# Kernel tuning notes

Hardware: AMD Instinct MI355X
Metric: run time of the kernel (lower is better)

The kernel has to match this reference:

```python
import jax, jax.numpy as jnp
import numpy as np

LATENT = 1024
HIDDEN = 4096
ENC = 1024
HEADS = 16
HEAD_DIM = LATENT // HEADS
B, SQ, SK = 4, 1024, 1024
EPS = 1e-5


def _linear(x, w, b):
    # torch nn.Linear: y = x @ w.T + b, w shape (out, in)
    return jnp.einsum('bsi,oi->bso', x, w) + b


def _mha(Q, K, wq, bq, wk, bk, wv, bv, wo, bo):
    Bq, Sq, _ = Q.shape
    Sk = K.shape[1]
    Qp = _linear(Q, wq, bq).reshape(Bq, Sq, HEADS, HEAD_DIM)
    Kp = _linear(K, wk, bk).reshape(Bq, Sk, HEADS, HEAD_DIM)
    Vp = _linear(K, wv, bv).reshape(Bq, Sk, HEADS, HEAD_DIM)
    # NOTE: original scales by 1/sqrt(latent_size), not 1/sqrt(head_dim)
    E = jnp.einsum('bqhd,bkhd->bhqk', Qp, Kp) / np.sqrt(LATENT).astype(np.float32)
    A = jax.nn.softmax(E, axis=-1)
    O = jnp.einsum('bhqk,bkhd->bqhd', A, Vp).reshape(Bq, Sq, LATENT)
    return _linear(O, wo, bo)


def _ln(x, g, b):
    mu = jnp.mean(x, axis=-1, keepdims=True)
    var = jnp.mean((x - mu) ** 2, axis=-1, keepdims=True)
    return (x - mu) * jax.lax.rsqrt(var + EPS) * g + b


def setup_inputs() -> dict:
    key = jax.random.key(0)
    ks = jax.random.split(key, 32)
    s = 0.02
    d = {
        'Q': jax.random.normal(ks[0], (B, SQ, LATENT), jnp.float32),
        'K': jax.random.normal(ks[1], (B, SK, ENC), jnp.float32),
        'a1_wq': jax.random.normal(ks[2], (LATENT, LATENT)) * s,
        'a1_bq': jnp.zeros((LATENT,)),
        'a1_wk': jax.random.normal(ks[3], (LATENT, LATENT)) * s,
        'a1_bk': jnp.zeros((LATENT,)),
        'a1_wv': jax.random.normal(ks[4], (LATENT, LATENT)) * s,
        'a1_bv': jnp.zeros((LATENT,)),
        'a1_wo': jax.random.normal(ks[5], (LATENT, LATENT)) * s,
        'a1_bo': jnp.zeros((LATENT,)),
        'a2_wq': jax.random.normal(ks[6], (LATENT, LATENT)) * s,
        'a2_bq': jnp.zeros((LATENT,)),
        'a2_wk': jax.random.normal(ks[7], (LATENT, ENC)) * s,
        'a2_bk': jnp.zeros((LATENT,)),
        'a2_wv': jax.random.normal(ks[8], (LATENT, ENC)) * s,
        'a2_bv': jnp.zeros((LATENT,)),
        'a2_wo': jax.random.normal(ks[9], (LATENT, LATENT)) * s,
        'a2_bo': jnp.zeros((LATENT,)),
        'fc_w1': jax.random.normal(ks[10], (HIDDEN, LATENT)) * s,
        'fc_b1': jnp.zeros((HIDDEN,)),
        'fc_w2': jax.random.normal(ks[11], (LATENT, HIDDEN)) * s,
        'fc_b2': jnp.zeros((LATENT,)),
        'ln0_g': jnp.ones((LATENT,)), 'ln0_b': jnp.zeros((LATENT,)),
        'ln1_g': jnp.ones((LATENT,)), 'ln1_b': jnp.zeros((LATENT,)),
        'ln2_g': jnp.ones((LATENT,)), 'ln2_b': jnp.zeros((LATENT,)),
    }
    return d


def reference(Q, K, a1_wq, a1_bq, a1_wk, a1_bk, a1_wv, a1_bv, a1_wo, a1_bo,
              a2_wq, a2_bq, a2_wk, a2_bk, a2_wv, a2_bv, a2_wo, a2_bo,
              fc_w1, fc_b1, fc_w2, fc_b2,
              ln0_g, ln0_b, ln1_g, ln1_b, ln2_g, ln2_b):
    # self-attention block
    A1 = _mha(Q, Q, a1_wq, a1_bq, a1_wk, a1_bk, a1_wv, a1_bv, a1_wo, a1_bo)
    X = _ln(Q + A1, ln0_g, ln0_b)
    # cross-attention block
    A2 = _mha(X, K, a2_wq, a2_bq, a2_wk, a2_bk, a2_wv, a2_bv, a2_wo, a2_bo)
    X = _ln(X + A2, ln1_g, ln1_b)
    # FFN: Linear -> ReLU -> Linear
    FC = _linear(jax.nn.relu(_linear(X, fc_w1, fc_b1)), fc_w2, fc_b2)
    X = _ln(X + FC, ln2_g, ln2_b)
    return X
```

## Files before the change

kernel.cpp:

```cpp
#include <hip/hip_runtime.h>
#include <hip/hip_bf16.h>
#include <math.h>

#define LATENT 1024
#define HIDDEN 4096
#define HEADS 16
#define HEAD_DIM 64
#define BATCH 4
#define SQL 1024
#define SKL 1024

typedef __bf16 bf16;
typedef __attribute__((ext_vector_type(4))) __bf16 bf16x4;
typedef __attribute__((ext_vector_type(8))) __bf16 bf16x8;
typedef __attribute__((ext_vector_type(4))) float f32x4;

#define MFMA16 __builtin_amdgcn_mfma_f32_16x16x32_bf16

__device__ __forceinline__ void async_ld16(const bf16* g, bf16* l) {
    __builtin_amdgcn_global_load_lds(
        (const __attribute__((address_space(1))) unsigned int*)g,
        (__attribute__((address_space(3))) unsigned int*)l,
        16, 0, 0);
}

__global__ void detect_dtype(const void* g, int* flag) {
    if (threadIdx.x == 0) *flag = (*(const float*)g == 1.0f) ? 1 : 0;
}

struct CanonArgs {
    const void* src[28];
    bf16* dst[28];
    int n[28];
};

__global__ __launch_bounds__(256) void canonicalize(CanonArgs a, const int* flagp) {
    const int buf = blockIdx.y;
    const int n = a.n[buf];
    const int i0 = (blockIdx.x * 256 + threadIdx.x) * 8;
    if (i0 >= n) return;
    bf16* dst = a.dst[buf];
    if (*flagp) {
        const float* s = (const float*)a.src[buf];
        float4 u0 = *(const float4*)(s + i0);
        float4 u1 = *(const float4*)(s + i0 + 4);
        bf16x8 o;
        o[0] = (bf16)u0.x; o[1] = (bf16)u0.y; o[2] = (bf16)u0.z; o[3] = (bf16)u0.w;
        o[4] = (bf16)u1.x; o[5] = (bf16)u1.y; o[6] = (bf16)u1.z; o[7] = (bf16)u1.w;
        *(bf16x8*)(dst + i0) = o;
    } else {
        *(bf16x8*)(dst + i0) = *(const bf16x8*)((const bf16*)a.src[buf] + i0);
    }
}

template<bool RELU>
__global__ __launch_bounds__(256, 2)
void gemm8(const bf16* __restrict__ A, const bf16* __restrict__ W,
           const bf16* __restrict__ bias,
           bf16* __restrict__ out0, bf16* __restrict__ out1, bf16* __restrict__ outT,
           int M, int N, int K, int nNormal, int ostride) {
    constexpr int AE   = 128 * 32;
    constexpr int BE   = 256 * 32;
    constexpr int BUFE = AE + BE;
    __shared__ alignas(16) bf16 smem[3 * BUFE];
    const int tid  = threadIdx.x;
    const int w    = tid >> 6;
    const int lane = tid & 63;
    const int quad = lane >> 4;
    const int l16  = lane & 15;
    const int wrr  = w >> 1, wcc = w & 1;
    const int nx  = gridDim.x;
    const int nwg = nx * gridDim.y;
    int bid = blockIdx.y * nx + blockIdx.x;
    bid = (bid & 7) * (nwg >> 3) + (bid >> 3);
    const int bm = (bid / nx) * 128;
    const int bn = (bid % nx) * 256;

    f32x4 acc[4][8] = {};

    const bf16* gsrc[6]; int loff[6];
#pragma unroll
    for (int i = 0; i < 6; ++i) {
        const int s = tid + i * 256;
        if (s < 512) {
            const int r = s >> 2, cs = s & 3;
            gsrc[i] = A + (long)(bm + r) * K + ((cs ^ ((r >> 1) & 3)) << 3);
            loff[i] = s * 8;
        } else {
            const int sb = s - 512;
            const int r = sb >> 2, cs = sb & 3;
            gsrc[i] = W + (long)(bn + r) * K + ((cs ^ ((r >> 1) & 3)) << 3);
            loff[i] = AE + sb * 8;
        }
    }

    int offA[4], offB[8];
#pragma unroll
    for (int i = 0; i < 4; ++i) {
        const int r = wrr * 64 + i * 16 + l16;
        offA[i] = r * 32 + ((quad ^ ((r >> 1) & 3)) << 3);
    }
#pragma unroll
    for (int j = 0; j < 8; ++j) {
        const int r = wcc * 128 + j * 16 + l16;
        offB[j] = AE + r * 32 + ((quad ^ ((r >> 1) & 3)) << 3);
    }

#define STAGE_W(dst, tt)                                                       \
    {                                                                          \
        _Pragma("unroll")                                                      \
        for (int i_ = 0; i_ < 6; ++i_)                                         \
            async_ld16(gsrc[i_] + (tt) * 32, (dst) + loff[i_]);                \
    }

    const int NK = K >> 5;
    bf16 *p0 = smem, *p1 = smem + BUFE, *p2 = smem + 2 * BUFE;
    STAGE_W(p0, 0);
    STAGE_W(p1, 1);
    __asm__ volatile("s_waitcnt vmcnt(6)" ::: "memory");
    __builtin_amdgcn_s_barrier();
    __builtin_amdgcn_sched_barrier(0);

    for (int t = 0; t < NK; ++t) {
        if (t + 2 < NK) STAGE_W(p2, t + 2);
        bf16x8 af[4], bfv[8];
#pragma unroll
        for (int i = 0; i < 4; ++i) af[i]  = *(const bf16x8*)&p0[offA[i]];
#pragma unroll
        for (int j = 0; j < 8; ++j) bfv[j] = *(const bf16x8*)&p0[offB[j]];
#pragma unroll
        for (int j = 0; j < 8; ++j)
#pragma unroll
            for (int i = 0; i < 4; ++i)
                acc[i][j] = MFMA16(af[i], bfv[j], acc[i][j], 0, 0, 0);
        if (t + 2 < NK) {
            __asm__ volatile("s_waitcnt vmcnt(6)" ::: "memory");
        } else if (t + 1 < NK) {
            __asm__ volatile("s_waitcnt vmcnt(0)" ::: "memory");
        }
        if (t + 1 < NK) {
            __builtin_amdgcn_s_barrier();
            __builtin_amdgcn_sched_barrier(0);
        }
        bf16* tp = p0; p0 = p1; p1 = p2; p2 = tp;
    }
#undef STAGE_W

    float bvv[8];
#pragma unroll
    for (int j = 0; j < 8; ++j) bvv[j] = (float)bias[bn + wcc * 128 + j * 16 + l16];

    if (bn < nNormal) {
#pragma unroll
        for (int j = 0; j < 8; ++j) {
            const int colj = bn + wcc * 128 + j * 16;
            bf16* basej = out0;
            int cb = colj;
            if (out1 && cb >= 1024) { basej = out1; cb -= 1024; }
#pragma unroll
            for (int i = 0; i < 4; ++i) {
#pragma unroll
                for (int r = 0; r < 4; ++r) {
                    const int row = bm + wrr * 64 + i * 16 + quad * 4 + r;
                    float v = acc[i][j][r] + bvv[j];
                    if (RELU) v = fmaxf(v, 0.f);
                    basej[(long)row * ostride + cb + l16] = (bf16)v;
                }
            }
        }
    } else {
        const int n0v = bn - nNormal;
        __syncthreads();
#pragma unroll
        for (int p = 0; p < 4; ++p) {
            if (p) __syncthreads();
            if (wcc == (p >> 1)) {
#pragma unroll
                for (int i = 0; i < 4; ++i)
#pragma unroll
                    for (int jl = 0; jl < 4; ++jl) {
                        const int j = (p & 1) * 4 + jl;
                        const int colL = jl * 16 + l16;
                        const int rowL = wrr * 64 + i * 16 + quad * 4;
                        bf16x4 pk;
#pragma unroll
                        for (int r = 0; r < 4; ++r) pk[r] = (bf16)(acc[i][j][r] + bvv[j]);
                        *(bf16x4*)&smem[colL * 136 + rowL] = pk;
                    }
            }
            __syncthreads();
#pragma unroll
            for (int k = 0; k < 8; ++k) {
                const int c = tid + k * 256;
                const int rT = c >> 5, ch = c & 31;
                *(bf16x4*)&outT[(long)(n0v + p * 64 + rT) * M + bm + ch * 4] =
                    *(const bf16x4*)&smem[rT * 136 + ch * 4];
            }
        }
    }
}

template<int BN, bool RELU>
__global__ __launch_bounds__(256, 2)
void gemm2(const bf16* __restrict__ A, const bf16* __restrict__ W,
           const bf16* __restrict__ bias,
           bf16* __restrict__ out0, bf16* __restrict__ out1, bf16* __restrict__ outT,
           int M, int N, int K, int nNormal, int ostride) {
    constexpr int WAVES_N = BN / 64;
    constexpr int WAVES_M = 4 / WAVES_N;
    constexpr int WM = 128 / WAVES_M;
    constexpr int MI = WM / 16;
    constexpr int BROWS = BN / 4;
    constexpr int BUFSZ = (128 + BN) * 64;
    __shared__ alignas(16) bf16 smem[2 * BUFSZ];
    const int tid  = threadIdx.x;
    const int w    = tid >> 6;
    const int lane = tid & 63;
    const int quad = lane >> 4;
    const int l16  = lane & 15;
    const int bm = blockIdx.y * 128;
    const int bn = blockIdx.x * BN;
    const int wr = w / WAVES_N, wc = w % WAVES_N;

    f32x4 acc[MI][4] = {};

    const int srow = lane >> 3;
    const int schk = (lane & 7) * 8;
    const bf16* Abase = A + (long)(bm + w * 32 + srow) * K + schk;
    const bf16* Wbase = W + (long)(bn + w * BROWS + srow) * K + schk;
    const int lAoff = (w * 32 + srow) * 64 + schk;
    const int lBoff = 128 * 64 + (w * BROWS + srow) * 64 + schk;

#define STAGE_G(bufp, kk)                                                      \
    {                                                                          \
        bf16* bb_ = smem + (bufp) * BUFSZ;                                     \
        _Pragma("unroll")                                                      \
        for (int i_ = 0; i_ < 4; ++i_)                                         \
            async_ld16(Abase + (kk) + (long)(i_ * 8) * K, bb_ + lAoff + i_ * 8 * 64); \
        _Pragma("unroll")                                                      \
        for (int i_ = 0; i_ < BROWS / 8; ++i_)                                 \
            async_ld16(Wbase + (kk) + (long)(i_ * 8) * K, bb_ + lBoff + i_ * 8 * 64); \
    }

    STAGE_G(0, 0);
    __asm__ volatile("s_waitcnt vmcnt(0)" ::: "memory");
    __builtin_amdgcn_s_barrier();
    __builtin_amdgcn_sched_barrier(0);

    int cur = 0;
    for (int k0 = 0; k0 < K; k0 += 64) {
        if (k0 + 64 < K) STAGE_G(cur ^ 1, k0 + 64);
        const bf16* lA = smem + cur * BUFSZ;
        const bf16* lB = lA + 128 * 64;
#pragma unroll
        for (int ks = 0; ks < 2; ++ks) {
            bf16x8 af[MI], bfv[4];
#pragma unroll
            for (int i = 0; i < MI; ++i)
                af[i] = *(const bf16x8*)&lA[(wr * WM + i * 16 + l16) * 64 + ks * 32 + quad * 8];
#pragma unroll
            for (int j = 0; j < 4; ++j)
                bfv[j] = *(const bf16x8*)&lB[(wc * 64 + j * 16 + l16) * 64 + ks * 32 + quad * 8];
#pragma unroll
            for (int i = 0; i < MI; ++i)
#pragma unroll
                for (int j = 0; j < 4; ++j)
                    acc[i][j] = MFMA16(af[i], bfv[j], acc[i][j], 0, 0, 0);
        }
        __asm__ volatile("s_waitcnt vmcnt(0)" ::: "memory");
        __builtin_amdgcn_s_barrier();
        __builtin_amdgcn_sched_barrier(0);
        cur ^= 1;
    }
#undef STAGE_G

    float bvv[4];
#pragma unroll
    for (int j = 0; j < 4; ++j) bvv[j] = (float)bias[bn + wc * 64 + j * 16 + l16];

    if (bn < nNormal) {
        bf16* base = out0;
        int colb = bn;
        if (out1 && colb >= 1024) { base = out1; colb -= 1024; }
#pragma unroll
        for (int i = 0; i < MI; ++i) {
#pragma unroll
            for (int r = 0; r < 4; ++r) {
                const int row = bm + wr * WM + i * 16 + quad * 4 + r;
#pragma unroll
                for (int j = 0; j < 4; ++j) {
                    float v = acc[i][j][r] + bvv[j];
                    if (RELU) v = fmaxf(v, 0.f);
                    base[(long)row * ostride + colb + wc * 64 + j * 16 + l16] = (bf16)v;
                }
            }
        }
    } else {
        const int n0v = bn - nNormal;
        __syncthreads();
#pragma unroll
        for (int p = 0; p < 2; ++p) {
            if (p) __syncthreads();
            if (wc == p) {
#pragma unroll
                for (int i = 0; i < MI; ++i)
#pragma unroll
                    for (int j = 0; j < 4; ++j) {
                        const int colL = j * 16 + l16;
                        const int rowL = wr * WM + i * 16 + quad * 4;
                        bf16x4 pk;
#pragma unroll
                        for (int r = 0; r < 4; ++r) pk[r] = (bf16)(acc[i][j][r] + bvv[j]);
                        *(bf16x4*)&smem[colL * 136 + rowL] = pk;
                    }
            }
            __syncthreads();
#pragma unroll
            for (int k = 0; k < 8; ++k) {
                const int c = tid + k * 256;
                const int rL = c >> 5, ch = c & 31;
                *(bf16x4*)&outT[(long)(n0v + p * 64 + rL) * M + bm + ch * 4] =
                    *(const bf16x4*)&smem[rL * 136 + ch * 4];
            }
        }
    }
}

__global__ __launch_bounds__(256, 3)
void attn2(const bf16* __restrict__ Qp, const bf16* __restrict__ Kp,
           const bf16* __restrict__ Vt, bf16* __restrict__ O) {
    __shared__ alignas(16) bf16 lQ[64 * 64];
    __shared__ alignas(16) bf16 lK[2][64 * 64];
    __shared__ alignas(16) bf16 lV[2][64 * 64];
    __shared__ alignas(16) bf16 lP[4][16 * 64];
    const int tid  = threadIdx.x;
    const int w    = tid >> 6;
    const int lane = tid & 63;
    const int quad = lane >> 4;
    const int l16  = lane & 15;
    const int b  = blockIdx.z;
    const int h  = blockIdx.y;
    const int q0 = blockIdx.x * 64;

#pragma unroll
    for (int s = 0; s < 2; ++s) {
        const int c = w * 128 + s * 64 + lane;
        const int row = c >> 3, ch = (c & 7) * 8;
        async_ld16(Qp + (long)(b * SQL + q0 + row) * LATENT + h * 64 + ch, lQ + c * 8);
    }
#define STAGE_KV(buf, kt)                                                        \
    {                                                                            \
        _Pragma("unroll")                                                        \
        for (int s = 0; s < 2; ++s) {                                            \
            const int c = w * 128 + s * 64 + lane;                               \
            const int row = c >> 3, ch = (c & 7) * 8;                            \
            async_ld16(Kp + (long)(b * SKL + (kt) * 64 + row) * LATENT + h * 64 + ch, \
                       &lK[buf][c * 8]);                                         \
            async_ld16(Vt + (long)(h * 64 + row) * (BATCH * SKL) + b * SKL + (kt) * 64 + ch, \
                       &lV[buf][c * 8]);                                         \
        }                                                                        \
    }
    STAGE_KV(0, 0);
    __syncthreads();

    bf16x8 aq[2];
    aq[0] = *(const bf16x8*)&lQ[(w * 16 + l16) * 64 + quad * 8];
    aq[1] = *(const bf16x8*)&lQ[(w * 16 + l16) * 64 + 32 + quad * 8];

    f32x4 o_acc[4] = {};
    float lsum[4] = {0.f, 0.f, 0.f, 0.f};

    for (int kt = 0; kt < SKL / 64; ++kt) {
        const int cur = kt & 1;
        if (kt < SKL / 64 - 1) STAGE_KV(cur ^ 1, kt + 1);

        f32x4 s4[4] = {};
#pragma unroll
        for (int ks = 0; ks < 2; ++ks)
#pragma unroll
            for (int j = 0; j < 4; ++j) {
                bf16x8 bk = *(const bf16x8*)&lK[cur][(j * 16 + l16) * 64 + ks * 32 + quad * 8];
                s4[j] = MFMA16(aq[ks], bk, s4[j], 0, 0, 0);
            }

#pragma unroll
        for (int r = 0; r < 4; ++r)
#pragma unroll
            for (int j = 0; j < 4; ++j) {
                const float p = __expf(s4[j][r] * 0.03125f);
                lsum[r] += p;
                lP[w][(quad * 4 + r) * 64 + j * 16 + l16] = (bf16)p;
            }
        __asm__ volatile("s_waitcnt lgkmcnt(0)" ::: "memory");

#pragma unroll
        for (int ks = 0; ks < 2; ++ks) {
            bf16x8 ap = *(const bf16x8*)&lP[w][l16 * 64 + ks * 32 + quad * 8];
#pragma unroll
            for (int j = 0; j < 4; ++j) {
                bf16x8 bv = *(const bf16x8*)&lV[cur][(j * 16 + l16) * 64 + ks * 32 + quad * 8];
                o_acc[j] = MFMA16(ap, bv, o_acc[j], 0, 0, 0);
            }
        }
        __syncthreads();
    }

#pragma unroll
    for (int r = 0; r < 4; ++r) {
#pragma unroll
        for (int off = 1; off <= 8; off <<= 1)
            lsum[r] += __shfl_xor(lsum[r], off, 64);
    }
#pragma unroll
    for (int r = 0; r < 4; ++r) {
        const float inv = 1.f / lsum[r];
        const int row = q0 + w * 16 + quad * 4 + r;
#pragma unroll
        for (int j = 0; j < 4; ++j)
            O[(long)(b * SQL + row) * LATENT + h * 64 + j * 16 + l16] = (bf16)(o_acc[j][r] * inv);
    }
#undef STAGE_KV
}

template<bool F32OUT>
__global__ __launch_bounds__(256)
void ln_kernel(const bf16* __restrict__ res, const bf16* __restrict__ y,
               const bf16* __restrict__ g, const bf16* __restrict__ bta,
               bf16* __restrict__ outres, void* __restrict__ outb) {
    const int row = blockIdx.x;
    const int tid = threadIdx.x;
    const long base = (long)row * LATENT;
    const int c = tid * 4;
    bf16x4 rv = *(const bf16x4*)&res[base + c];
    bf16x4 yv = *(const bf16x4*)&y[base + c];
    float x[4];
    float s1 = 0.f, s2 = 0.f;
#pragma unroll
    for (int i = 0; i < 4; ++i) {
        float v = (float)rv[i] + (float)yv[i];
        x[i] = v; s1 += v; s2 += v * v;
    }
#pragma unroll
    for (int off = 32; off >= 1; off >>= 1) {
        s1 += __shfl_xor(s1, off, 64);
        s2 += __shfl_xor(s2, off, 64);
    }
    __shared__ float ps1[4], ps2[4];
    const int w = tid >> 6, lane = tid & 63;
    if (lane == 0) { ps1[w] = s1; ps2[w] = s2; }
    __syncthreads();
    s1 = ps1[0] + ps1[1] + ps1[2] + ps1[3];
    s2 = ps2[0] + ps2[1] + ps2[2] + ps2[3];
    const float mu = s1 * (1.f / LATENT);
    const float var = s2 * (1.f / LATENT) - mu * mu;
    const float rstd = rsqrtf(var + 1e-5f);
    bf16x4 gv = *(const bf16x4*)&g[c];
    bf16x4 bv = *(const bf16x4*)&bta[c];
    float o[4];
#pragma unroll
    for (int i = 0; i < 4; ++i)
        o[i] = (x[i] - mu) * rstd * (float)gv[i] + (float)bv[i];
    if (F32OUT) {
        float4 f; f.x = o[0]; f.y = o[1]; f.z = o[2]; f.w = o[3];
        *(float4*)&((float*)outb)[base + c] = f;
    } else {
        bf16x4 bo;
#pragma unroll
        for (int i = 0; i < 4; ++i) bo[i] = (bf16)o[i];
        *(bf16x4*)&((bf16*)outb)[base + c] = bo;
        if (outres) *(bf16x4*)&outres[base + c] = bo;
    }
}

extern "C" void kernel_launch(void* const* d_in, const int* in_sizes, int n_in,
                              void* d_out, int out_size, void* d_ws, size_t ws_size,
                              hipStream_t stream) {
    char* ws = (char*)d_ws;

    static const int order[28] = {2, 4, 6, 3, 5, 7, 12, 14, 13, 15,
                                  0, 1, 8, 9, 10, 11, 16, 17, 18, 19,
                                  20, 21, 22, 23, 24, 25, 26, 27};
    size_t coff[28];
    size_t cur = 256;
    for (int k = 0; k < 28; ++k) {
        const int i = order[k];
        coff[i] = cur;
        cur += (((size_t)in_sizes[i] * 2) + 255) & ~(size_t)255;
    }
    const size_t canon_end = (cur + 255) & ~(size_t)255;
    const size_t MB8 = 8ull << 20;
    const size_t need = canon_end + 7 * MB8;
    const bool full = ws_size >= need;

    const bf16* cv[28];
    if (full) {
        int* flag = (int*)ws;
        detect_dtype<<<dim3(1), dim3(64), 0, stream>>>(d_in[22], flag);
        CanonArgs ca;
        for (int i = 0; i < 28; ++i) {
            ca.src[i] = d_in[i];
            ca.dst[i] = (bf16*)(ws + coff[i]);
            ca.n[i]   = in_sizes[i];
            cv[i]     = (const bf16*)(ws + coff[i]);
        }
        canonicalize<<<dim3(2048, 28), dim3(256), 0, stream>>>(ca, flag);
    } else {
        for (int i = 0; i < 28; ++i) cv[i] = (const bf16*)d_in[i];
    }

    const size_t base = full ? canon_end : 0;
    bf16* Xres = (bf16*)(ws + base);
    bf16* Yf   = (bf16*)(ws + base + 1 * MB8);
    bf16* Xb   = (bf16*)(ws + base + 2 * MB8);
    bf16* Qp   = (bf16*)(ws + base + 3 * MB8);
    bf16* Kp   = (bf16*)(ws + base + 4 * MB8);
    bf16* Vt   = (bf16*)(ws + base + 5 * MB8);
    bf16* AttO = (bf16*)(ws + base + 6 * MB8);
    bf16* H    = Qp;

    const bf16 *Qc = cv[0], *Kc = cv[1];
    const int M = BATCH * SQL;
    dim3 blk(256);
    dim3 ga(SQL / 64, HEADS, BATCH);

    gemm8<false><<<dim3(3072 / 256, M / 128), blk, 0, stream>>>(
        Qc, cv[2], cv[3], Qp, Kp, Vt, M, 3072, LATENT, 2048, 1024);
    attn2<<<ga, blk, 0, stream>>>(Qp, Kp, Vt, AttO);
    gemm2<64, false><<<dim3(1024 / 64, M / 128), blk, 0, stream>>>(
        AttO, cv[8], cv[9], Yf, nullptr, nullptr, M, 1024, LATENT, 1024, 1024);
    ln_kernel<false><<<dim3(M), blk, 0, stream>>>(Qc, Yf, cv[22], cv[23], Xres, Xb);

    gemm2<64, false><<<dim3(1024 / 64, M / 128), blk, 0, stream>>>(
        Xb, cv[10], cv[11], Qp, nullptr, nullptr, M, 1024, LATENT, 1024, 1024);
    gemm8<false><<<dim3(2048 / 256, M / 128), blk, 0, stream>>>(
        Kc, cv[12], cv[13], Kp, nullptr, Vt, M, 2048, LATENT, 1024, 1024);
    attn2<<<ga, blk, 0, stream>>>(Qp, Kp, Vt, AttO);
    gemm2<64, false><<<dim3(1024 / 64, M / 128), blk, 0, stream>>>(
        AttO, cv[16], cv[17], Yf, nullptr, nullptr, M, 1024, LATENT, 1024, 1024);
    ln_kernel<false><<<dim3(M), blk, 0, stream>>>(Xres, Yf, cv[24], cv[25], Xres, Xb);

    gemm8<true><<<dim3(4096 / 256, M / 128), blk, 0, stream>>>(
        Xb, cv[18], cv[19], H, nullptr, nullptr, M, HIDDEN, LATENT, 4096, 4096);
    gemm2<64, false><<<dim3(1024 / 64, M / 128), blk, 0, stream>>>(
        H, cv[20], cv[21], Yf, nullptr, nullptr, M, 1024, HIDDEN, 1024, 1024);
    ln_kernel<true><<<dim3(M), blk, 0, stream>>>(Xres, Yf, cv[26], cv[27], nullptr, d_out);
}
```

Measured before the change: 515.8 us.

## XOR-swizzle shared-memory tiles in GEMM and attention to remove bank conflicts

Applies an XOR swizzle to the 16-byte chunk index of every LDS tile (GEMM A/W tiles, attention Q/K/V/P tiles), on both the async global-to-LDS writes and the MFMA fragment reads. The 64-element row stride previously made the bf16x8 fragment reads hit the same LDS banks, and the swizzle spreads them out. The GEMM staging is also reorganised so all 256 threads cover A and W slots uniformly with precomputed source pointers. It adds s_setprio around the MFMA sections in attention. Any mismatch between the write and read swizzle would corrupt results.

```diff
diff --git a/kernel.cpp b/kernel.cpp
--- a/kernel.cpp
+++ b/kernel.cpp
@@ -210,7 +210,9 @@
     constexpr int WAVES_M = 4 / WAVES_N;
     constexpr int WM = 128 / WAVES_M;
     constexpr int MI = WM / 16;
-    constexpr int BROWS = BN / 4;
+    constexpr int AE    = 128 * 64;
+    constexpr int SLOTS = (128 + BN) * 8;
+    constexpr int LPT   = SLOTS / 256;
     constexpr int BUFSZ = (128 + BN) * 64;
     __shared__ alignas(16) bf16 smem[2 * BUFSZ];
     const int tid  = threadIdx.x;
@@ -221,25 +223,40 @@
     const int bm = blockIdx.y * 128;
     const int bn = blockIdx.x * BN;
     const int wr = w / WAVES_N, wc = w % WAVES_N;
+    const int pp = l16 >> 1;
 
     f32x4 acc[MI][4] = {};
 
-    const int srow = lane >> 3;
-    const int schk = (lane & 7) * 8;
-    const bf16* Abase = A + (long)(bm + w * 32 + srow) * K + schk;
-    const bf16* Wbase = W + (long)(bn + w * BROWS + srow) * K + schk;
-    const int lAoff = (w * 32 + srow) * 64 + schk;
-    const int lBoff = 128 * 64 + (w * BROWS + srow) * 64 + schk;
+    const bf16* gsrc[LPT]; int loff[LPT];
+#pragma unroll
+    for (int i = 0; i < LPT; ++i) {
+        const int s = tid + i * 256;
+        if (s < 1024) {
+            const int r = s >> 3, cs = s & 7;
+            gsrc[i] = A + (long)(bm + r) * K + ((cs ^ ((r >> 1) & 7)) << 3);
+            loff[i] = s * 8;
+        } else {
+            const int sb = s - 1024;
+            const int r = sb >> 3, cs = sb & 7;
+            gsrc[i] = W + (long)(bn + r) * K + ((cs ^ ((r >> 1) & 7)) << 3);
+            loff[i] = AE + sb * 8;
+        }
+    }
+
+    int offA[MI], offB[4];
+#pragma unroll
+    for (int i = 0; i < MI; ++i)
+        offA[i] = (wr * WM + i * 16 + l16) * 64 + ((quad ^ pp) << 3);
+#pragma unroll
+    for (int j = 0; j < 4; ++j)
+        offB[j] = AE + (wc * 64 + j * 16 + l16) * 64 + ((quad ^ pp) << 3);
 
 #define STAGE_G(bufp, kk)                                                      \
     {                                                                          \
         bf16* bb_ = smem + (bufp) * BUFSZ;                                     \
         _Pragma("unroll")                                                      \
-        for (int i_ = 0; i_ < 4; ++i_)                                         \
-            async_ld16(Abase + (kk) + (long)(i_ * 8) * K, bb_ + lAoff + i_ * 8 * 64); \
-        _Pragma("unroll")                                                      \
-        for (int i_ = 0; i_ < BROWS / 8; ++i_)                                 \
-            async_ld16(Wbase + (kk) + (long)(i_ * 8) * K, bb_ + lBoff + i_ * 8 * 64); \
+        for (int i_ = 0; i_ < LPT; ++i_)                                       \
+            async_ld16(gsrc[i_] + (kk), bb_ + loff[i_]);                       \
     }
 
     STAGE_G(0, 0);
@@ -250,17 +267,16 @@
     int cur = 0;
     for (int k0 = 0; k0 < K; k0 += 64) {
         if (k0 + 64 < K) STAGE_G(cur ^ 1, k0 + 64);
-        const bf16* lA = smem + cur * BUFSZ;
-        const bf16* lB = lA + 128 * 64;
+        const bf16* lbuf = smem + cur * BUFSZ;
 #pragma unroll
         for (int ks = 0; ks < 2; ++ks) {
             bf16x8 af[MI], bfv[4];
 #pragma unroll
             for (int i = 0; i < MI; ++i)
-                af[i] = *(const bf16x8*)&lA[(wr * WM + i * 16 + l16) * 64 + ks * 32 + quad * 8];
+                af[i] = *(const bf16x8*)&lbuf[offA[i] ^ (ks << 5)];
 #pragma unroll
             for (int j = 0; j < 4; ++j)
-                bfv[j] = *(const bf16x8*)&lB[(wc * 64 + j * 16 + l16) * 64 + ks * 32 + quad * 8];
+                bfv[j] = *(const bf16x8*)&lbuf[offB[j] ^ (ks << 5)];
 #pragma unroll
             for (int i = 0; i < MI; ++i)
 #pragma unroll
@@ -338,6 +354,7 @@
     const int lane = tid & 63;
     const int quad = lane >> 4;
     const int l16  = lane & 15;
+    const int pp   = l16 >> 1;
     const int b  = blockIdx.z;
     const int h  = blockIdx.y;
     const int q0 = blockIdx.x * 64;
@@ -345,7 +362,8 @@
 #pragma unroll
     for (int s = 0; s < 2; ++s) {
         const int c = w * 128 + s * 64 + lane;
-        const int row = c >> 3, ch = (c & 7) * 8;
+        const int row = c >> 3;
+        const int ch = (((c & 7) ^ ((row >> 1) & 7)) << 3);
         async_ld16(Qp + (long)(b * SQL + q0 + row) * LATENT + h * 64 + ch, lQ + c * 8);
     }
 #define STAGE_KV(buf, kt)                                                        \
@@ -353,7 +371,8 @@
         _Pragma("unroll")                                                        \
         for (int s = 0; s < 2; ++s) {                                            \
             const int c = w * 128 + s * 64 + lane;                               \
-            const int row = c >> 3, ch = (c & 7) * 8;                            \
+            const int row = c >> 3;                                              \
+            const int ch = (((c & 7) ^ ((row >> 1) & 7)) << 3);                  \
             async_ld16(Kp + (long)(b * SKL + (kt) * 64 + row) * LATENT + h * 64 + ch, \
                        &lK[buf][c * 8]);                                         \
             async_ld16(Vt + (long)(h * 64 + row) * (BATCH * SKL) + b * SKL + (kt) * 64 + ch, \
@@ -363,9 +382,15 @@
     STAGE_KV(0, 0);
     __syncthreads();
 
+    const int aqoff = (w * 16 + l16) * 64 + ((quad ^ pp) << 3);
     bf16x8 aq[2];
-    aq[0] = *(const bf16x8*)&lQ[(w * 16 + l16) * 64 + quad * 8];
-    aq[1] = *(const bf16x8*)&lQ[(w * 16 + l16) * 64 + 32 + quad * 8];
+    aq[0] = *(const bf16x8*)&lQ[aqoff];
+    aq[1] = *(const bf16x8*)&lQ[aqoff ^ 32];
+    int kvb[4];
+#pragma unroll
+    for (int j = 0; j < 4; ++j)
+        kvb[j] = (j * 16 + l16) * 64 + ((quad ^ pp) << 3);
+    const int apb = l16 * 64 + ((quad ^ pp) << 3);
 
     f32x4 o_acc[4] = {};
     float lsum[4] = {0.f, 0.f, 0.f, 0.f};
@@ -375,33 +400,39 @@
         if (kt < SKL / 64 - 1) STAGE_KV(cur ^ 1, kt + 1);
 
         f32x4 s4[4] = {};
+        __builtin_amdgcn_s_setprio(1);
 #pragma unroll
         for (int ks = 0; ks < 2; ++ks)
 #pragma unroll
             for (int j = 0; j < 4; ++j) {
-                bf16x8 bk = *(const bf16x8*)&lK[cur][(j * 16 + l16) * 64 + ks * 32 + quad * 8];
+                bf16x8 bk = *(const bf16x8*)&lK[cur][kvb[j] ^ (ks << 5)];
                 s4[j] = MFMA16(aq[ks], bk, s4[j], 0, 0, 0);
             }
-
-#pragma unroll
-        for (int r = 0; r < 4; ++r)
+        __builtin_amdgcn_s_setprio(0);
+
+#pragma unroll
+        for (int r = 0; r < 4; ++r) {
+            const int psx = ((quad * 2 + (r >> 1)) & 7) << 3;
 #pragma unroll
             for (int j = 0; j < 4; ++j) {
                 const float p = __expf(s4[j][r] * 0.03125f);
                 lsum[r] += p;
-                lP[w][(quad * 4 + r) * 64 + j * 16 + l16] = (bf16)p;
-            }
+                lP[w][(quad * 4 + r) * 64 + ((j * 16 + l16) ^ psx)] = (bf16)p;
+            }
+        }
         __asm__ volatile("s_waitcnt lgkmcnt(0)" ::: "memory");
 
+        __builtin_amdgcn_s_setprio(1);
 #pragma unroll
         for (int ks = 0; ks < 2; ++ks) {
-            bf16x8 ap = *(const bf16x8*)&lP[w][l16 * 64 + ks * 32 + quad * 8];
+            bf16x8 ap = *(const bf16x8*)&lP[w][apb ^ (ks << 5)];
 #pragma unroll
             for (int j = 0; j < 4; ++j) {
-                bf16x8 bv = *(const bf16x8*)&lV[cur][(j * 16 + l16) * 64 + ks * 32 + quad * 8];
+                bf16x8 bv = *(const bf16x8*)&lV[cur][kvb[j] ^ (ks << 5)];
                 o_acc[j] = MFMA16(ap, bv, o_acc[j], 0, 0, 0);
             }
         }
+        __builtin_amdgcn_s_setprio(0);
         __syncthreads();
     }
 
```

Result: faster. 480.7 us (-6.8%).
